# Kernel optimization log

Hardware: AMD Instinct MI355X
Metric: run time of the kernel (lower is better)

## Reference

```python
import jax, jax.numpy as jnp
import numpy as np

H, FF = 4096, 14336   # hidden size, SwiGLU intermediate size
B, S = 4, 2048        # batch, sequence length


def setup_inputs() -> dict:
    key = jax.random.key(0)
    ks = jax.random.split(key, 7)
    x = jax.random.normal(ks[0], (B, S, H), dtype=jnp.float32)
    # Ternary weights: values in {-1, 0, +1}
    gate_t = jax.random.randint(ks[1], (FF, H), -1, 2, dtype=jnp.int32)
    up_t = jax.random.randint(ks[2], (FF, H), -1, 2, dtype=jnp.int32)
    down_t = jax.random.randint(ks[3], (H, FF), -1, 2, dtype=jnp.int32)
    # Per-output-row scales (positive, realistic quantization scale magnitudes)
    gate_s = jax.random.uniform(ks[4], (FF,), jnp.float32, 0.01, 0.1)
    up_s = jax.random.uniform(ks[5], (FF,), jnp.float32, 0.01, 0.1)
    down_s = jax.random.uniform(ks[6], (H,), jnp.float32, 0.01, 0.1)
    return {"x": x, "gate_t": gate_t, "up_t": up_t, "down_t": down_t,
            "gate_s": gate_s, "up_s": up_s, "down_s": down_s}


def reference(x, gate_t, up_t, down_t, gate_s, up_s, down_s):
    # SwiGLU forward with on-the-fly ternary dequant, matching
    # TernaryExpertModule.forward (output_proj=None).
    Bb, Ss, Hh = x.shape
    x_flat = x.reshape(Bb * Ss, Hh)                         # [BS, H]
    gate_w = gate_t.astype(jnp.float32) * gate_s[:, None]   # [FF, H]
    up_w = up_t.astype(jnp.float32) * up_s[:, None]         # [FF, H]
    down_w = down_t.astype(jnp.float32) * down_s[:, None]   # [H, FF]
    gate_out = x_flat @ gate_w.T                            # [BS, FF]
    up_out = x_flat @ up_w.T                                # [BS, FF]
    hidden = jax.nn.silu(gate_out) * up_out                 # [BS, FF]
    out_flat = hidden @ down_w.T                            # [BS, H]
    return out_flat.reshape(Bb, Ss, -1)
```

## Files before the change

### kernel.cpp

```cpp
#include <hip/hip_runtime.h>
#include <stdint.h>

#define H_DIM   4096
#define FF_DIM  14336
#define M_TOK   8192
#define KC1     (H_DIM / 32)
#define KC2     (FF_DIM / 32)
#define KC1_8   (H_DIM / 64)

typedef unsigned short ushort_t;
typedef __attribute__((ext_vector_type(8))) short  bf16x8;
typedef __attribute__((ext_vector_type(4))) float  f32x4;
typedef __attribute__((ext_vector_type(4))) int    i32x4;

__device__ __forceinline__ unsigned short f2bf(float f) {
    union { float f; uint32_t u; } v; v.f = f;
    uint32_t r = v.u + 0x7FFFu + ((v.u >> 16) & 1u);
    return (unsigned short)(r >> 16);
}
__device__ __forceinline__ unsigned short t2bf(int v) {
    unsigned int mag = (v & 1) ? 0x3F80u : 0u;
    unsigned int sgn = ((unsigned int)v >> 16) & 0x8000u;
    return (unsigned short)(mag | sgn);
}
__device__ __forceinline__ bf16x8 pack_f8(f32x4 a, f32x4 b) {
    bf16x8 o;
    o[0]=(short)f2bf(a[0]); o[1]=(short)f2bf(a[1]); o[2]=(short)f2bf(a[2]); o[3]=(short)f2bf(a[3]);
    o[4]=(short)f2bf(b[0]); o[5]=(short)f2bf(b[1]); o[6]=(short)f2bf(b[2]); o[7]=(short)f2bf(b[3]);
    return o;
}
__device__ __forceinline__ bf16x8 pack_t8(i32x4 a, i32x4 b) {
    bf16x8 o;
    o[0]=(short)t2bf(a[0]); o[1]=(short)t2bf(a[1]); o[2]=(short)t2bf(a[2]); o[3]=(short)t2bf(a[3]);
    o[4]=(short)t2bf(b[0]); o[5]=(short)t2bf(b[1]); o[6]=(short)t2bf(b[2]); o[7]=(short)t2bf(b[3]);
    return o;
}
__device__ __forceinline__ int pack4(int a, int b, int c, int d) {
    return (a & 255) | ((b & 255) << 8) | ((c & 255) << 16) | ((d & 255) << 24);
}

#define GLDS16(gp, lp) __builtin_amdgcn_global_load_lds( \
    (__attribute__((address_space(1))) void*)(gp),       \
    (__attribute__((address_space(3))) void*)(lp), 16, 0, 0)

#define WAITVM8 asm volatile("s_waitcnt vmcnt(8)" ::: "memory")
#define WAITVM4 asm volatile("s_waitcnt vmcnt(4)" ::: "memory")
#define WAITVM0 asm volatile("s_waitcnt vmcnt(0)" ::: "memory")
#define SBAR    asm volatile("s_barrier" ::: "memory")


template<int K, bool TERN>
__global__ __launch_bounds__(256)
void k_cvt_lds(const void* __restrict__ inv, unsigned short* __restrict__ out) {
    constexpr int KC = K / 32;
    constexpr int CP = K / 64;
    __shared__ int sm[128][68];
    const int b   = blockIdx.x;
    const int t   = b / CP;
    const int cp  = b % CP;
    const int tid = threadIdx.x;
    const int rr  = tid >> 4;
    const int c4  = (tid & 15) * 4;
    const int k0  = cp * 64;

    const int* in = (const int*)inv;
    #pragma unroll
    for (int p = 0; p < 8; ++p) {
        const int row = p * 16 + rr;
        *(i32x4*)&sm[row][c4] = *(const i32x4*)(in + (size_t)(t * 128 + row) * K + k0 + c4);
    }
    __syncthreads();
    #pragma unroll
    for (int p = 0; p < 4; ++p) {
        const int idx = p * 256 + tid;
        const int cc  = idx >> 9;
        const int f   = (idx >> 6) & 7;
        const int l   = idx & 63;
        const int row = f * 16 + (l & 15);
        const int kl  = cc * 32 + (l >> 4) * 8;
        bf16x8 o;
        if (TERN) {
            i32x4 a = *(const i32x4*)&sm[row][kl];
            i32x4 bq = *(const i32x4*)&sm[row][kl + 4];
            o = pack_t8(a, bq);
        } else {
            f32x4 a = *(const f32x4*)&sm[row][kl];
            f32x4 bq = *(const f32x4*)&sm[row][kl + 4];
            o = pack_f8(a, bq);
        }
        *(bf16x8*)(out + (((size_t)t * KC + (cp * 2 + cc)) * 8 + f) * 512 + (size_t)l * 8) = o;
    }
}

__global__ __launch_bounds__(256)
void k_amax(const float* __restrict__ x, float* __restrict__ sx, float* __restrict__ rsx) {
    const int row  = blockIdx.x * 4 + (threadIdx.x >> 6);
    const int lane = threadIdx.x & 63;
    const f32x4* p = (const f32x4*)(x + (size_t)row * H_DIM);
    float m = 0.f;
    #pragma unroll 4
    for (int i = lane; i < H_DIM / 4; i += 64) {
        f32x4 v = p[i];
        m = fmaxf(m, fmaxf(fmaxf(fabsf(v[0]), fabsf(v[1])), fmaxf(fabsf(v[2]), fabsf(v[3]))));
    }
    #pragma unroll
    for (int o = 32; o; o >>= 1) m = fmaxf(m, __shfl_xor(m, o, 64));
    if (lane == 0) {
        sx[row]  = m * (1.f / 127.f);
        rsx[row] = m > 0.f ? 127.f / m : 0.f;
    }
}

template<int K, bool TERN>
__global__ __launch_bounds__(256)
void k_cvt_i8(const void* __restrict__ inv, const float* __restrict__ rsx,
              char* __restrict__ out) {
    constexpr int CP = K / 64;
    __shared__ int sm[128][68];
    const int b   = blockIdx.x;
    const int t   = b / CP;
    const int cp  = b % CP;
    const int tid = threadIdx.x;
    const int rr  = tid >> 4;
    const int c4  = (tid & 15) * 4;

    const int* in = (const int*)inv;
    #pragma unroll
    for (int p = 0; p < 8; ++p) {
        const int row = p * 16 + rr;
        *(i32x4*)&sm[row][c4] = *(const i32x4*)(in + (size_t)(t * 128 + row) * K + cp * 64 + c4);
    }
    __syncthreads();
    #pragma unroll
    for (int p = 0; p < 2; ++p) {
        const int pos = p * 256 + tid;
        const int f = pos >> 6, l = pos & 63;
        const int row = f * 16 + (l & 15);
        const int kb  = (l >> 4) * 16;
        i32x4 o;
        if constexpr (TERN) {
            #pragma unroll
            for (int q = 0; q < 4; ++q)
                o[q] = pack4(sm[row][kb + q * 4], sm[row][kb + q * 4 + 1],
                             sm[row][kb + q * 4 + 2], sm[row][kb + q * 4 + 3]);
        } else {
            const float rs = rsx[t * 128 + row];
            #pragma unroll
            for (int q = 0; q < 4; ++q) {
                const float* fp = (const float*)&sm[row][kb + q * 4];
                o[q] = pack4(__float2int_rn(fp[0] * rs), __float2int_rn(fp[1] * rs),
                             __float2int_rn(fp[2] * rs), __float2int_rn(fp[3] * rs));
            }
        }
        *(i32x4*)(out + ((size_t)t * CP + cp) * 8192 + f * 1024 + (size_t)l * 16) = o;
    }
}

__global__ __launch_bounds__(512, 2)
void k_gemm1_i8(const char* __restrict__ xq,
                const char* __restrict__ gq, const char* __restrict__ uq,
                const float* __restrict__ sxp,
                const float* __restrict__ gs, const float* __restrict__ us,
                ushort_t* __restrict__ hid)
{
    __shared__ char lds[131072];
    const int tid  = threadIdx.x;
    const int lane = tid & 63;
    const int wv   = tid >> 6;
    const int wr   = wv >> 1;
    const int wc   = wv & 1;
    const int l15  = lane & 15;
    const int lq   = lane >> 4;

    const int bid = blockIdx.x;
    const int bmt = bid & 31;
    const int bnt = bid >> 5;

    const char* xa0 = xq + (size_t)(bmt * 2)     * KC1_8 * 8192;
    const char* xa1 = xq + (size_t)(bmt * 2 + 1) * KC1_8 * 8192;
    const char* gbb = gq + (size_t)bnt * KC1_8 * 8192;
    const char* ubb = uq + (size_t)bnt * KC1_8 * 8192;

    i32x4 accg[4][4] = {};
    i32x4 accu[4][4] = {};

    #pragma unroll
    for (int h = 0; h < 3; ++h) {
        char* sl = lds + h * 32768;
        GLDS16(xa0 + (size_t)h * 8192 + tid * 16, sl + tid * 16);
        GLDS16(xa1 + (size_t)h * 8192 + tid * 16, sl + 8192 + tid * 16);
        GLDS16(gbb + (size_t)h * 8192 + tid * 16, sl + 16384 + tid * 16);
        GLDS16(ubb + (size_t)h * 8192 + tid * 16, sl + 24576 + tid * 16);
    }

#define G1I(WAITOP, DO_ISSUE)                                                      \
  {                                                                                \
    char* slot = lds + (H & 3) * 32768;                                            \
    const char* Ab = slot + (wr >> 1) * 8192 + ((wr & 1) * 4) * 1024 + lane * 16;  \
    const char* Gb = slot + 16384 + (wc * 4) * 1024 + lane * 16;                   \
    const char* Ub = slot + 24576 + (wc * 4) * 1024 + lane * 16;                   \
    WAITOP;                                                                        \
    SBAR;                                                                          \
    i32x4 af[4], gf[4], uf[4];                                                     \
    _Pragma("unroll")                                                              \
    for (int m = 0; m < 4; m++) af[m] = *(const i32x4*)(Ab + m * 1024);            \
    _Pragma("unroll")                                                              \
    for (int n = 0; n < 4; n++) gf[n] = *(const i32x4*)(Gb + n * 1024);            \
    if (DO_ISSUE) {                                                                \
      const int Hp = H + 3;                                                        \
      char* sp = lds + (Hp & 3) * 32768;                                           \
      GLDS16(xa0 + (size_t)Hp * 8192 + tid * 16, sp + tid * 16);                   \
      GLDS16(xa1 + (size_t)Hp * 8192 + tid * 16, sp + 8192 + tid * 16);            \
    }                                                                              \
    __builtin_amdgcn_s_setprio(1);                                                 \
    _Pragma("unroll")                                                              \
    for (int m = 0; m < 4; m++)                                                    \
      _Pragma("unroll")                                                            \
      for (int n = 0; n < 4; n++)                                                  \
        accg[m][n] = __builtin_amdgcn_mfma_i32_16x16x64_i8(af[m], gf[n], accg[m][n], 0, 0, 0); \
    __builtin_amdgcn_s_setprio(0);                                                 \
    SBAR;                                                                          \
    _Pragma("unroll")                                                              \
    for (int n = 0; n < 4; n++) uf[n] = *(const i32x4*)(Ub + n * 1024);            \
    if (DO_ISSUE) {                                                                \
      const int Hp = H + 3;                                                        \
      char* sp = lds + (Hp & 3) * 32768;                                           \
      GLDS16(gbb + (size_t)Hp * 8192 + tid * 16, sp + 16384 + tid * 16);           \
      GLDS16(ubb + (size_t)Hp * 8192 + tid * 16, sp + 24576 + tid * 16);           \
    }                                                                              \
    __builtin_amdgcn_s_setprio(1);                                                 \
    _Pragma("unroll")                                                              \
    for (int m = 0; m < 4; m++)                                                    \
      _Pragma("unroll")                                                            \
      for (int n = 0; n < 4; n++)                                                  \
        accu[m][n] = __builtin_amdgcn_mfma_i32_16x16x64_i8(af[m], uf[n], accu[m][n], 0, 0, 0); \
    __builtin_amdgcn_s_setprio(0);                                                 \
  }

    int H = 0;
    for (; H < KC1_8 - 3; ++H) G1I(WAITVM8, 1);
    G1I(WAITVM8, 0); ++H;
    G1I(WAITVM4, 0); ++H;
    G1I(WAITVM0, 0);
#undef G1I

    const int bm0 = bmt * 256;
    const int bn0 = bnt * 128;
    float sxv[4][4];
    #pragma unroll
    for (int m = 0; m < 4; m++) {
        const int rb = bm0 + wr * 64 + m * 16 + lq * 4;
        #pragma unroll
        for (int r = 0; r < 4; r++) sxv[m][r] = sxp[rb + r];
    }
    #pragma unroll
    for (int n = 0; n < 4; n++) {
        const int gcol = bn0 + wc * 64 + n * 16 + l15;
        const float sg = gs[gcol];
        const float su = us[gcol];
        const int c  = gcol >> 5;
        const int lp = ((gcol & 31) >> 3) * 16;
        const int e  = gcol & 7;
        #pragma unroll
        for (int m = 0; m < 4; m++) {
            const int rb = bm0 + wr * 64 + m * 16 + lq * 4;
            #pragma unroll
            for (int r = 0; r < 4; r++) {
                const int row = rb + r;
                float g = (float)accg[m][n][r] * (sxv[m][r] * sg);
                float u = (float)accu[m][n][r] * (sxv[m][r] * su);
                float hv = g * (1.0f / (1.0f + __expf(-g))) * u;
                const int t = row >> 7;
                const int f = (row >> 4) & 7;
                const int l = (row & 15) + lp;
                hid[(((size_t)t * KC2 + c) * 8 + f) * 512 + l * 8 + e] = f2bf(hv);
            }
        }
    }
}

__global__ __launch_bounds__(512, 2)
void k_gemm2_8p(const ushort_t* __restrict__ hid, const ushort_t* __restrict__ db,
                const float* __restrict__ dsc, float* __restrict__ out)
{
    __shared__ ushort_t lds[65536];
    const int tid  = threadIdx.x;
    const int lane = tid & 63;
    const int wv   = tid >> 6;
    const int wr   = wv >> 2;
    const int wc   = wv & 3;
    const int l15  = lane & 15;
    const int lq   = lane >> 4;

    const int bid = blockIdx.x;
    const int bmt = bid & 31;
    const int bnt = bid >> 5;

    const ushort_t* ha0 = hid + ((size_t)(bmt * 2)     * KC2) * 4096;
    const ushort_t* ha1 = hid + ((size_t)(bmt * 2 + 1) * KC2) * 4096;
    const ushort_t* db0 = db  + ((size_t)(bnt * 2)     * KC2) * 4096;
    const ushort_t* db1 = db  + ((size_t)(bnt * 2 + 1) * KC2) * 4096;

    f32x4 acc[8][4] = {};

    #pragma unroll
    for (int h = 0; h < 3; ++h) {
        ushort_t* sl = lds + h * 16384;
        GLDS16(ha0 + (size_t)h * 4096 + tid * 8, sl + tid * 8);
        GLDS16(ha1 + (size_t)h * 4096 + tid * 8, sl + 4096 + tid * 8);
        GLDS16(db0 + (size_t)h * 4096 + tid * 8, sl + 8192 + tid * 8);
        GLDS16(db1 + (size_t)h * 4096 + tid * 8, sl + 12288 + tid * 8);
    }

#define G2_HALF(WAITOP, DO_ISSUE)                                                  \
  {                                                                                \
    ushort_t* slot = lds + (H & 3) * 16384;                                        \
    const ushort_t* Ab = slot + wr * 4096 + lane * 8;                              \
    const ushort_t* Bb = slot + 8192 + (wc >> 1) * 4096 + ((wc & 1) * 4) * 512 + lane * 8; \
    WAITOP;                                                                        \
    SBAR;                                                                          \
    bf16x8 af[4], bfv[4];                                                          \
    _Pragma("unroll")                                                              \
    for (int m = 0; m < 4; m++) af[m] = *(const bf16x8*)(Ab + m * 512);            \
    _Pragma("unroll")                                                              \
    for (int n = 0; n < 4; n++) bfv[n] = *(const bf16x8*)(Bb + n * 512);           \
    if (DO_ISSUE) {                                                                \
      const int Hp = H + 3;                                                        \
      ushort_t* sp = lds + (Hp & 3) * 16384;                                       \
      GLDS16(ha0 + (size_t)Hp * 4096 + tid * 8, sp + tid * 8);                     \
      GLDS16(ha1 + (size_t)Hp * 4096 + tid * 8, sp + 4096 + tid * 8);              \
    }                                                                              \
    __builtin_amdgcn_s_setprio(1);                                                 \
    _Pragma("unroll")                                                              \
    for (int m = 0; m < 4; m++)                                                    \
      _Pragma("unroll")                                                            \
      for (int n = 0; n < 4; n++)                                                  \
        acc[m][n] = __builtin_amdgcn_mfma_f32_16x16x32_bf16(af[m], bfv[n], acc[m][n], 0, 0, 0); \
    __builtin_amdgcn_s_setprio(0);                                                 \
    SBAR;                                                                          \
    bf16x8 af2[4];                                                                 \
    _Pragma("unroll")                                                              \
    for (int m = 0; m < 4; m++) af2[m] = *(const bf16x8*)(Ab + (4 + m) * 512);     \
    if (DO_ISSUE) {                                                                \
      const int Hp = H + 3;                                                        \
      ushort_t* sp = lds + (Hp & 3) * 16384;                                       \
      GLDS16(db0 + (size_t)Hp * 4096 + tid * 8, sp + 8192 + tid * 8);              \
      GLDS16(db1 + (size_t)Hp * 4096 + tid * 8, sp + 12288 + tid * 8);             \
    }                                                                              \
    __builtin_amdgcn_s_setprio(1);                                                 \
    _Pragma("unroll")                                                              \
    for (int m = 0; m < 4; m++)                                                    \
      _Pragma("unroll")                                                            \
      for (int n = 0; n < 4; n++)                                                  \
        acc[4 + m][n] = __builtin_amdgcn_mfma_f32_16x16x32_bf16(af2[m], bfv[n], acc[4 + m][n], 0, 0, 0); \
    __builtin_amdgcn_s_setprio(0);                                                 \
  }

    int H = 0;
    for (; H < KC2 - 3; ++H) G2_HALF(WAITVM8, 1);
    G2_HALF(WAITVM8, 0); ++H;
    G2_HALF(WAITVM4, 0); ++H;
    G2_HALF(WAITVM0, 0);
#undef G2_HALF

    const int bm0 = bmt * 256;
    const int bn0 = bnt * 256;
    #pragma unroll
    for (int n = 0; n < 4; n++) {
        const int gcol = bn0 + wc * 64 + n * 16 + l15;
        const float sd = dsc[gcol];
        #pragma unroll
        for (int m = 0; m < 8; m++) {
            const int grow = bm0 + wr * 128 + m * 16 + lq * 4;
            #pragma unroll
            for (int r = 0; r < 4; r++)
                out[(size_t)(grow + r) * H_DIM + gcol] = acc[m][n][r] * sd;
        }
    }
}

__device__ __forceinline__ void ds_write_frag(ushort_t* buf, int crow, int ccol,
                                              bf16x8 lo, bf16x8 hi) {
    int f  = crow >> 4;
    int la = (crow & 15) + (((ccol)     & 31) >> 3) * 16;
    int lb = (crow & 15) + (((ccol + 8) & 31) >> 3) * 16;
    *(bf16x8*)&buf[f * 512 + la * 8] = lo;
    *(bf16x8*)&buf[f * 512 + lb * 8] = hi;
}

template<bool PREA>
__global__ __launch_bounds__(256, 2)
void k_gemm1_fb(const float* __restrict__ xf, const ushort_t* __restrict__ xb,
                const int* __restrict__ gt, const int* __restrict__ ut,
                const float* __restrict__ gs, const float* __restrict__ us,
                ushort_t* __restrict__ hid)
{
    __shared__ ushort_t As[4096];
    __shared__ ushort_t Gs[4096];
    __shared__ ushort_t Us[4096];

    const int tid  = threadIdx.x;
    const int lane = tid & 63;
    const int wv   = tid >> 6;
    const int wr   = wv >> 1;
    const int wc   = wv & 1;
    const int l15  = lane & 15;
    const int lq   = lane >> 4;

    const int bid = blockIdx.x;
    const int bmt = bid & 63;
    const int bnt = bid >> 6;
    const int bm0 = bmt * 128;
    const int bn0 = bnt * 128;

    f32x4 accg[4][4] = {};
    f32x4 accu[4][4] = {};

    const ushort_t* pa = PREA ? xb + (size_t)bmt * KC1 * 4096 : nullptr;
    const int crow = tid >> 1;
    const int ccol = (tid & 1) * 16;

    for (int kc = 0; kc < KC1; kc++) {
        __syncthreads();
        const int k0 = kc * 32;
        if constexpr (PREA) {
            GLDS16(pa + tid * 8,        &As[tid * 8]);
            GLDS16(pa + tid * 8 + 2048, &As[tid * 8 + 2048]);
        } else {
            const float* xa = xf + (size_t)(bm0 + crow) * H_DIM + k0 + ccol;
            f32x4 a0 = ((const f32x4*)xa)[0], a1 = ((const f32x4*)xa)[1];
            f32x4 a2 = ((const f32x4*)xa)[2], a3 = ((const f32x4*)xa)[3];
            ds_write_frag(As, crow, ccol, pack_f8(a0, a1), pack_f8(a2, a3));
        }
        {
            const size_t wo = (size_t)(bn0 + crow) * H_DIM + k0 + ccol;
            const i32x4* gp = (const i32x4*)(gt + wo);
            i32x4 g0 = gp[0], g1 = gp[1], g2 = gp[2], g3 = gp[3];
            ds_write_frag(Gs, crow, ccol, pack_t8(g0, g1), pack_t8(g2, g3));
            const i32x4* up = (const i32x4*)(ut + wo);
            i32x4 u0 = up[0], u1 = up[1], u2 = up[2], u3 = up[3];
            ds_write_frag(Us, crow, ccol, pack_t8(u0, u1), pack_t8(u2, u3));
        }
        __syncthreads();

        bf16x8 af[4], gf[4], uf[4];
        #pragma unroll
        for (int m = 0; m < 4; m++)
            af[m] = *(const bf16x8*)&As[(wr * 4 + m) * 512 + lane * 8];
        #pragma unroll
        for (int n = 0; n < 4; n++) {
            gf[n] = *(const bf16x8*)&Gs[(wc * 4 + n) * 512 + lane * 8];
            uf[n] = *(const bf16x8*)&Us[(wc * 4 + n) * 512 + lane * 8];
        }
        #pragma unroll
        for (int m = 0; m < 4; m++)
            #pragma unroll
            for (int n = 0; n < 4; n++) {
                accg[m][n] = __builtin_amdgcn_mfma_f32_16x16x32_bf16(af[m], gf[n], accg[m][n], 0, 0, 0);
                accu[m][n] = __builtin_amdgcn_mfma_f32_16x16x32_bf16(af[m], uf[n], accu[m][n], 0, 0, 0);
            }
        if constexpr (PREA) pa += 4096;
    }

    #pragma unroll
    for (int n = 0; n < 4; n++) {
        const int gcol = bn0 + wc * 64 + n * 16 + l15;
        const float sg = gs[gcol];
        const float su = us[gcol];
        const int c  = gcol >> 5;
        const int lp = ((gcol & 31) >> 3) * 16;
        const int e  = gcol & 7;
        #pragma unroll
        for (int m = 0; m < 4; m++) {
            const int rb = bm0 + wr * 64 + m * 16 + lq * 4;
            #pragma unroll
            for (int r = 0; r < 4; r++) {
                const int row = rb + r;
                float g = accg[m][n][r] * sg;
                float u = accu[m][n][r] * su;
                float hv = g * (1.0f / (1.0f + __expf(-g))) * u;
                const int t = row >> 7;
                const int f = (row >> 4) & 7;
                const int l = (row & 15) + lp;
                hid[(((size_t)t * KC2 + c) * 8 + f) * 512 + l * 8 + e] = f2bf(hv);
            }
        }
    }
}

__global__ __launch_bounds__(256, 2)
void k_gemm2_fb(const ushort_t* __restrict__ hid, const int* __restrict__ dt,
                const float* __restrict__ dsc, float* __restrict__ out)
{
    __shared__ ushort_t As[4096];
    __shared__ ushort_t Bs[4096];

    const int tid  = threadIdx.x;
    const int lane = tid & 63;
    const int wv   = tid >> 6;
    const int wr   = wv >> 1;
    const int wc   = wv & 1;
    const int l15  = lane & 15;
    const int lq   = lane >> 4;

    const int bid = blockIdx.x;
    const int bmt = bid & 63;
    const int bnt = bid >> 6;
    const int bm0 = bmt * 128;
    const int bn0 = bnt * 128;

    f32x4 acc[4][4] = {};
    const ushort_t* pa = hid + (size_t)bmt * KC2 * 4096;
    const int crow = tid >> 1;
    const int ccol = (tid & 1) * 16;

    for (int kc = 0; kc < KC2; kc++) {
        __syncthreads();
        GLDS16(pa + tid * 8,        &As[tid * 8]);
        GLDS16(pa + tid * 8 + 2048, &As[tid * 8 + 2048]);
        {
            const i32x4* dp = (const i32x4*)(dt + (size_t)(bn0 + crow) * FF_DIM + kc * 32 + ccol);
            i32x4 d0 = dp[0], d1 = dp[1], d2 = dp[2], d3 = dp[3];
            ds_write_frag(Bs, crow, ccol, pack_t8(d0, d1), pack_t8(d2, d3));
        }
        __syncthreads();

        bf16x8 af[4], bfr[4];
        #pragma unroll
        for (int m = 0; m < 4; m++)
            af[m] = *(const bf16x8*)&As[(wr * 4 + m) * 512 + lane * 8];
        #pragma unroll
        for (int n = 0; n < 4; n++)
            bfr[n] = *(const bf16x8*)&Bs[(wc * 4 + n) * 512 + lane * 8];
        #pragma unroll
        for (int m = 0; m < 4; m++)
            #pragma unroll
            for (int n = 0; n < 4; n++)
                acc[m][n] = __builtin_amdgcn_mfma_f32_16x16x32_bf16(af[m], bfr[n], acc[m][n], 0, 0, 0);
        pa += 4096;
    }

    #pragma unroll
    for (int n = 0; n < 4; n++) {
        const int gcol = bn0 + wc * 64 + n * 16 + l15;
        const float sd = dsc[gcol];
        #pragma unroll
        for (int m = 0; m < 4; m++) {
            const int grow = bm0 + wr * 64 + m * 16 + lq * 4;
            #pragma unroll
            for (int r = 0; r < 4; r++)
                out[(size_t)(grow + r) * H_DIM + gcol] = acc[m][n][r] * sd;
        }
    }
}

extern "C" void kernel_launch(void* const* d_in, const int* in_sizes, int n_in,
                              void* d_out, int out_size, void* d_ws, size_t ws_size,
                              hipStream_t stream) {
    const float* xf  = (const float*)d_in[0];
    const int*   gt  = (const int*)d_in[1];
    const int*   ut  = (const int*)d_in[2];
    const int*   dt  = (const int*)d_in[3];
    const float* gsc = (const float*)d_in[4];
    const float* usc = (const float*)d_in[5];
    const float* dsc = (const float*)d_in[6];
    float* out = (float*)d_out;

    const size_t HID_B = (size_t)M_TOK * FF_DIM * 2;
    const size_t DB_B  = (size_t)FF_DIM * H_DIM * 2;
    const size_t G8_B  = (size_t)FF_DIM * H_DIM;
    const size_t U8_B  = (size_t)FF_DIM * H_DIM;
    const size_t X8_B  = (size_t)M_TOK * H_DIM;
    const size_t SX_B  = (size_t)M_TOK * 4;
    const size_t XB_B  = (size_t)M_TOK * H_DIM * 2;

    char* base = (char*)d_ws;
    ushort_t* hid = (ushort_t*)base;
    ushort_t* dbp = (ushort_t*)(base + HID_B);
    char*     g8  = base + HID_B + DB_B;
    char*     u8  = g8 + G8_B;
    char*     x8  = u8 + U8_B;
    float*    sxp = (float*)(x8 + X8_B);
    float*    rsx = sxp + M_TOK;
    ushort_t* xbp = (ushort_t*)(base + HID_B);

    const bool has_w  = ws_size >= HID_B + DB_B + G8_B + U8_B + X8_B + 2 * SX_B;
    const bool has_xb = ws_size >= HID_B + XB_B;

    if (has_w) {
        k_amax<<<M_TOK / 4, 256, 0, stream>>>(xf, sxp, rsx);
        k_cvt_i8<H_DIM,  false><<<(M_TOK / 128) * (H_DIM / 64), 256, 0, stream>>>(xf, rsx, x8);
        k_cvt_i8<H_DIM,  true ><<<(FF_DIM / 128) * (H_DIM / 64), 256, 0, stream>>>(gt, nullptr, g8);
        k_cvt_i8<H_DIM,  true ><<<(FF_DIM / 128) * (H_DIM / 64), 256, 0, stream>>>(ut, nullptr, u8);
        k_cvt_lds<FF_DIM, true><<<(H_DIM / 128) * (FF_DIM / 64), 256, 0, stream>>>(dt, dbp);

        k_gemm1_i8<<<32 * 112, 512, 0, stream>>>(x8, g8, u8, sxp, gsc, usc, hid);
        k_gemm2_8p<<<32 * 16, 512, 0, stream>>>(hid, dbp, dsc, out);
    } else {
        const int grid1 = 64 * 112;
        const int grid2 = 64 * 32;
        if (has_xb) {
            k_cvt_lds<H_DIM, false><<<(M_TOK / 128) * (H_DIM / 64), 256, 0, stream>>>(xf, xbp);
            k_gemm1_fb<true><<<grid1, 256, 0, stream>>>(nullptr, xbp, gt, ut, gsc, usc, hid);
        } else {
            k_gemm1_fb<false><<<grid1, 256, 0, stream>>>(xf, nullptr, gt, ut, gsc, usc, hid);
        }
        k_gemm2_fb<<<grid2, 256, 0, stream>>>(hid, dt, dsc, out);
    }
}
```

Baseline: 1.723 ms.

## Switch gate/up int8 GEMM to 32x32x32 MFMA with matching operand layout

Replaces the 16x16x64 int8 MFMA tiles in the fused gate/up GEMM with 32x32x32 MFMA tiles. The int8 conversion kernel's packed output layout is changed to match the 32-row fragment format. The A fragments for the next k-step are prefetched from LDS into registers during the current step, and the pipeline waits on fewer outstanding loads. The aim is fewer MFMA issues and LDS reads per output, plus hiding LDS latency, at the cost of a new epilogue row mapping and per-element scale loads.

After: 1.814 ms. +5.3%, slower.

```diff
diff --git a/kernel.cpp b/kernel.cpp
--- a/kernel.cpp
+++ b/kernel.cpp
@@ -6,12 +6,14 @@
 #define M_TOK   8192
 #define KC1     (H_DIM / 32)
 #define KC2     (FF_DIM / 32)
-#define KC1_8   (H_DIM / 64)
+#define NC1     (H_DIM / 64)
+#define CPX     (H_DIM / 32)
 
 typedef unsigned short ushort_t;
-typedef __attribute__((ext_vector_type(8))) short  bf16x8;
-typedef __attribute__((ext_vector_type(4))) float  f32x4;
-typedef __attribute__((ext_vector_type(4))) int    i32x4;
+typedef __attribute__((ext_vector_type(8)))  short bf16x8;
+typedef __attribute__((ext_vector_type(4)))  float f32x4;
+typedef __attribute__((ext_vector_type(4)))  int   i32x4;
+typedef __attribute__((ext_vector_type(16))) int   i32x16;
 
 __device__ __forceinline__ unsigned short f2bf(float f) {
     union { float f; uint32_t u; } v; v.f = f;
@@ -115,11 +117,11 @@
 __global__ __launch_bounds__(256)
 void k_cvt_i8(const void* __restrict__ inv, const float* __restrict__ rsx,
               char* __restrict__ out) {
-    constexpr int CP = K / 64;
+    constexpr int CP = K / 32;
     __shared__ int sm[128][68];
     const int b   = blockIdx.x;
-    const int t   = b / CP;
-    const int cp  = b % CP;
+    const int t   = b / (K / 64);
+    const int cp  = b % (K / 64);
     const int tid = threadIdx.x;
     const int rr  = tid >> 4;
     const int c4  = (tid & 15) * 4;
@@ -134,9 +136,11 @@
     #pragma unroll
     for (int p = 0; p < 2; ++p) {
         const int pos = p * 256 + tid;
-        const int f = pos >> 6, l = pos & 63;
-        const int row = f * 16 + (l & 15);
-        const int kb  = (l >> 4) * 16;
+        const int cc  = pos >> 8;
+        const int f   = (pos >> 6) & 3;
+        const int l   = pos & 63;
+        const int row = f * 32 + (l & 31);
+        const int kb  = cc * 32 + (l >> 5) * 16;
         i32x4 o;
         if constexpr (TERN) {
             #pragma unroll
@@ -152,7 +156,7 @@
                              __float2int_rn(fp[2] * rs), __float2int_rn(fp[3] * rs));
             }
         }
-        *(i32x4*)(out + ((size_t)t * CP + cp) * 8192 + f * 1024 + (size_t)l * 16) = o;
+        *(i32x4*)(out + ((size_t)(t * CP + cp * 2 + cc) * 4 + f) * 1024 + (size_t)l * 16) = o;
     }
 }
 
@@ -169,106 +173,111 @@
     const int wv   = tid >> 6;
     const int wr   = wv >> 1;
     const int wc   = wv & 1;
-    const int l15  = lane & 15;
-    const int lq   = lane >> 4;
+    const int l31  = lane & 31;
+    const int lhi  = lane >> 5;
 
     const int bid = blockIdx.x;
     const int bmt = bid & 31;
     const int bnt = bid >> 5;
 
-    const char* xa0 = xq + (size_t)(bmt * 2)     * KC1_8 * 8192;
-    const char* xa1 = xq + (size_t)(bmt * 2 + 1) * KC1_8 * 8192;
-    const char* gbb = gq + (size_t)bnt * KC1_8 * 8192;
-    const char* ubb = uq + (size_t)bnt * KC1_8 * 8192;
-
-    i32x4 accg[4][4] = {};
-    i32x4 accu[4][4] = {};
-
-    #pragma unroll
-    for (int h = 0; h < 3; ++h) {
-        char* sl = lds + h * 32768;
-        GLDS16(xa0 + (size_t)h * 8192 + tid * 16, sl + tid * 16);
-        GLDS16(xa1 + (size_t)h * 8192 + tid * 16, sl + 8192 + tid * 16);
-        GLDS16(gbb + (size_t)h * 8192 + tid * 16, sl + 16384 + tid * 16);
-        GLDS16(ubb + (size_t)h * 8192 + tid * 16, sl + 24576 + tid * 16);
-    }
-
-#define G1I(WAITOP, DO_ISSUE)                                                      \
-  {                                                                                \
-    char* slot = lds + (H & 3) * 32768;                                            \
-    const char* Ab = slot + (wr >> 1) * 8192 + ((wr & 1) * 4) * 1024 + lane * 16;  \
-    const char* Gb = slot + 16384 + (wc * 4) * 1024 + lane * 16;                   \
-    const char* Ub = slot + 24576 + (wc * 4) * 1024 + lane * 16;                   \
-    WAITOP;                                                                        \
-    SBAR;                                                                          \
-    i32x4 af[4], gf[4], uf[4];                                                     \
-    _Pragma("unroll")                                                              \
-    for (int m = 0; m < 4; m++) af[m] = *(const i32x4*)(Ab + m * 1024);            \
-    _Pragma("unroll")                                                              \
-    for (int n = 0; n < 4; n++) gf[n] = *(const i32x4*)(Gb + n * 1024);            \
-    if (DO_ISSUE) {                                                                \
-      const int Hp = H + 3;                                                        \
-      char* sp = lds + (Hp & 3) * 32768;                                           \
-      GLDS16(xa0 + (size_t)Hp * 8192 + tid * 16, sp + tid * 16);                   \
-      GLDS16(xa1 + (size_t)Hp * 8192 + tid * 16, sp + 8192 + tid * 16);            \
-    }                                                                              \
-    __builtin_amdgcn_s_setprio(1);                                                 \
-    _Pragma("unroll")                                                              \
-    for (int m = 0; m < 4; m++)                                                    \
-      _Pragma("unroll")                                                            \
-      for (int n = 0; n < 4; n++)                                                  \
-        accg[m][n] = __builtin_amdgcn_mfma_i32_16x16x64_i8(af[m], gf[n], accg[m][n], 0, 0, 0); \
-    __builtin_amdgcn_s_setprio(0);                                                 \
-    SBAR;                                                                          \
-    _Pragma("unroll")                                                              \
-    for (int n = 0; n < 4; n++) uf[n] = *(const i32x4*)(Ub + n * 1024);            \
-    if (DO_ISSUE) {                                                                \
-      const int Hp = H + 3;                                                        \
-      char* sp = lds + (Hp & 3) * 32768;                                           \
-      GLDS16(gbb + (size_t)Hp * 8192 + tid * 16, sp + 16384 + tid * 16);           \
-      GLDS16(ubb + (size_t)Hp * 8192 + tid * 16, sp + 24576 + tid * 16);           \
-    }                                                                              \
-    __builtin_amdgcn_s_setprio(1);                                                 \
-    _Pragma("unroll")                                                              \
-    for (int m = 0; m < 4; m++)                                                    \
-      _Pragma("unroll")                                                            \
-      for (int n = 0; n < 4; n++)                                                  \
-        accu[m][n] = __builtin_amdgcn_mfma_i32_16x16x64_i8(af[m], uf[n], accu[m][n], 0, 0, 0); \
-    __builtin_amdgcn_s_setprio(0);                                                 \
+    const char* xa0  = xq + (size_t)(2 * bmt)     * CPX * 4096;
+    const char* xa1  = xq + (size_t)(2 * bmt + 1) * CPX * 4096;
+    const char* srcA = (tid < 256 ? xa0 : xa1 - 4096) + tid * 16;
+    const char* gbb  = gq + (size_t)bnt * CPX * 4096;
+    const char* ubb  = uq + (size_t)bnt * CPX * 4096;
+
+    i32x16 accg[2][2] = {};
+    i32x16 accu[2][2] = {};
+    i32x4  af[2][2], afn[2][2];
+
+#define STAGE1(h) { char* sl_ = lds + ((h) & 3) * 32768;                     \
+    GLDS16(srcA + (size_t)(h) * 8192,           sl_ + tid * 16);             \
+    GLDS16(srcA + (size_t)(h) * 8192 + 4096,    sl_ + 8192  + tid * 16);     \
+    GLDS16(gbb  + (size_t)(h) * 8192 + tid * 16, sl_ + 16384 + tid * 16);    \
+    GLDS16(ubb  + (size_t)(h) * 8192 + tid * 16, sl_ + 24576 + tid * 16); }
+
+    STAGE1(0); STAGE1(1); STAGE1(2);
+    WAITVM8;
+    SBAR;
+    #pragma unroll
+    for (int c2 = 0; c2 < 2; ++c2)
+        #pragma unroll
+        for (int i = 0; i < 2; ++i)
+            af[c2][i] = *(const i32x4*)(lds + c2 * 8192 + (wr * 2 + i) * 1024 + lane * 16);
+
+#define G1BODY(WAITOP, DO_STAGE, DO_AFN)                                            \
+  {                                                                                 \
+    char* slot = lds + (H & 3) * 32768;                                             \
+    WAITOP;                                              \
+    SBAR;               \
+    if (DO_STAGE) STAGE1(H + 3);                                                    \
+    i32x4 gf[2][2], uf[2][2];                                                       \
+    _Pragma("unroll")                                                               \
+    for (int c2 = 0; c2 < 2; ++c2)                                                  \
+      _Pragma("unroll")                                                             \
+      for (int n = 0; n < 2; ++n) {                                                 \
+        gf[c2][n] = *(const i32x4*)(slot + 16384 + c2 * 4096 + (wc * 2 + n) * 1024 + lane * 16); \
+        uf[c2][n] = *(const i32x4*)(slot + 24576 + c2 * 4096 + (wc * 2 + n) * 1024 + lane * 16); \
+      }                                                                             \
+    if (DO_AFN) {                                                                   \
+      char* sn = lds + ((H + 1) & 3) * 32768;                                       \
+      _Pragma("unroll")                                                             \
+      for (int c2 = 0; c2 < 2; ++c2)                                                \
+        _Pragma("unroll")                                                           \
+        for (int i = 0; i < 2; ++i)                                                 \
+          afn[c2][i] = *(const i32x4*)(sn + c2 * 8192 + (wr * 2 + i) * 1024 + lane * 16); \
+    }                                                                               \
+    __builtin_amdgcn_s_setprio(1);                                                  \
+    _Pragma("unroll")                                                               \
+    for (int c2 = 0; c2 < 2; ++c2)                                                  \
+      _Pragma("unroll")                                                             \
+      for (int i = 0; i < 2; ++i)                                                   \
+        _Pragma("unroll")                                                           \
+        for (int n = 0; n < 2; ++n)                                                 \
+          accg[i][n] = __builtin_amdgcn_mfma_i32_32x32x32_i8(af[c2][i], gf[c2][n], accg[i][n], 0, 0, 0); \
+    _Pragma("unroll")                                                               \
+    for (int c2 = 0; c2 < 2; ++c2)                                                  \
+      _Pragma("unroll")                                                             \
+      for (int i = 0; i < 2; ++i)                                                   \
+        _Pragma("unroll")                                                           \
+        for (int n = 0; n < 2; ++n)                                                 \
+          accu[i][n] = __builtin_amdgcn_mfma_i32_32x32x32_i8(af[c2][i], uf[c2][n], accu[i][n], 0, 0, 0); \
+    __builtin_amdgcn_s_setprio(0);                                                  \
+    if (DO_AFN) {                                                                   \
+      _Pragma("unroll")                                                             \
+      for (int c2 = 0; c2 < 2; ++c2)                                                \
+        _Pragma("unroll")                                                           \
+        for (int i = 0; i < 2; ++i) af[c2][i] = afn[c2][i];                         \
+    }                                                                               \
   }
 
     int H = 0;
-    for (; H < KC1_8 - 3; ++H) G1I(WAITVM8, 1);
-    G1I(WAITVM8, 0); ++H;
-    G1I(WAITVM4, 0); ++H;
-    G1I(WAITVM0, 0);
-#undef G1I
+    for (; H < NC1 - 3; ++H) G1BODY(WAITVM4, 1, 1);
+    G1BODY(WAITVM4, 0, 1); ++H;
+    G1BODY(WAITVM0, 0, 1); ++H;
+    G1BODY(WAITVM0, 0, 0);
+#undef G1BODY
+#undef STAGE1
 
     const int bm0 = bmt * 256;
     const int bn0 = bnt * 128;
-    float sxv[4][4];
-    #pragma unroll
-    for (int m = 0; m < 4; m++) {
-        const int rb = bm0 + wr * 64 + m * 16 + lq * 4;
-        #pragma unroll
-        for (int r = 0; r < 4; r++) sxv[m][r] = sxp[rb + r];
-    }
-    #pragma unroll
-    for (int n = 0; n < 4; n++) {
-        const int gcol = bn0 + wc * 64 + n * 16 + l15;
-        const float sg = gs[gcol];
-        const float su = us[gcol];
-        const int c  = gcol >> 5;
-        const int lp = ((gcol & 31) >> 3) * 16;
-        const int e  = gcol & 7;
-        #pragma unroll
-        for (int m = 0; m < 4; m++) {
-            const int rb = bm0 + wr * 64 + m * 16 + lq * 4;
-            #pragma unroll
-            for (int r = 0; r < 4; r++) {
-                const int row = rb + r;
-                float g = (float)accg[m][n][r] * (sxv[m][r] * sg);
-                float u = (float)accu[m][n][r] * (sxv[m][r] * su);
+    #pragma unroll
+    for (int i = 0; i < 2; ++i) {
+        #pragma unroll
+        for (int n = 0; n < 2; ++n) {
+            const int col = bn0 + wc * 64 + n * 32 + l31;
+            const float sg = gs[col];
+            const float su = us[col];
+            const int c  = col >> 5;
+            const int lp = ((col & 31) >> 3) * 16;
+            const int e  = col & 7;
+            #pragma unroll
+            for (int reg = 0; reg < 16; ++reg) {
+                const int row32 = (reg & 3) + 8 * (reg >> 2) + 4 * lhi;
+                const int row = bm0 + wr * 64 + i * 32 + row32;
+                const float sx = sxp[row];
+                float g = (float)accg[i][n][reg] * (sx * sg);
+                float u = (float)accu[i][n][reg] * (sx * su);
                 float hv = g * (1.0f / (1.0f + __expf(-g))) * u;
                 const int t = row >> 7;
                 const int f = (row >> 4) & 7;
```

## Switch gemm1 int8 pipeline from 4-slot triple-prefetch to double buffering

Applied to the files above, without the earlier changes.

Replaces the four-slot LDS ring, which prefetched three K-chunks ahead and split the issue of x and gate/up loads across two barrier phases, with a two-slot double buffer that prefetches one chunk ahead. LDS use halves to 64 KB, which could let more blocks fit per CU alongside the 512-thread launch bounds of 2. The cost is a shallower prefetch distance, so global-memory latency is hidden less, plus a trailing barrier added each iteration.

Measured after the change: 1.778 ms. 3.2% more time.

```diff
diff --git a/kernel.cpp b/kernel.cpp
--- a/kernel.cpp
+++ b/kernel.cpp
@@ -6,12 +6,12 @@
 #define M_TOK   8192
 #define KC1     (H_DIM / 32)
 #define KC2     (FF_DIM / 32)
-#define KC1_8   (H_DIM / 64)
+#define NC1     (H_DIM / 64)
 
 typedef unsigned short ushort_t;
-typedef __attribute__((ext_vector_type(8))) short  bf16x8;
-typedef __attribute__((ext_vector_type(4))) float  f32x4;
-typedef __attribute__((ext_vector_type(4))) int    i32x4;
+typedef __attribute__((ext_vector_type(8)))  short bf16x8;
+typedef __attribute__((ext_vector_type(4)))  float f32x4;
+typedef __attribute__((ext_vector_type(4)))  int   i32x4;
 
 __device__ __forceinline__ unsigned short f2bf(float f) {
     union { float f; uint32_t u; } v; v.f = f;
@@ -43,10 +43,10 @@
     (__attribute__((address_space(1))) void*)(gp),       \
     (__attribute__((address_space(3))) void*)(lp), 16, 0, 0)
 
-#define WAITVM8 asm volatile("s_waitcnt vmcnt(8)" ::: "memory")
-#define WAITVM4 asm volatile("s_waitcnt vmcnt(4)" ::: "memory")
-#define WAITVM0 asm volatile("s_waitcnt vmcnt(0)" ::: "memory")
-#define SBAR    asm volatile("s_barrier" ::: "memory")
+#define WAITVM8  asm volatile("s_waitcnt vmcnt(8)" ::: "memory")
+#define WAITVM4  asm volatile("s_waitcnt vmcnt(4)" ::: "memory")
+#define WAITVM0  asm volatile("s_waitcnt vmcnt(0)" ::: "memory")
+#define SBAR     asm volatile("s_barrier" ::: "memory")
 
 
 template<int K, bool TERN>
@@ -163,7 +163,7 @@
                 const float* __restrict__ gs, const float* __restrict__ us,
                 ushort_t* __restrict__ hid)
 {
-    __shared__ char lds[131072];
+    __shared__ char lds[65536];
     const int tid  = threadIdx.x;
     const int lane = tid & 63;
     const int wv   = tid >> 6;
@@ -176,73 +176,58 @@
     const int bmt = bid & 31;
     const int bnt = bid >> 5;
 
-    const char* xa0 = xq + (size_t)(bmt * 2)     * KC1_8 * 8192;
-    const char* xa1 = xq + (size_t)(bmt * 2 + 1) * KC1_8 * 8192;
-    const char* gbb = gq + (size_t)bnt * KC1_8 * 8192;
-    const char* ubb = uq + (size_t)bnt * KC1_8 * 8192;
+    const char* xa0 = xq + (size_t)(bmt * 2)     * NC1 * 8192;
+    const char* xa1 = xq + (size_t)(bmt * 2 + 1) * NC1 * 8192;
+    const char* gbb = gq + (size_t)bnt * NC1 * 8192;
+    const char* ubb = uq + (size_t)bnt * NC1 * 8192;
 
     i32x4 accg[4][4] = {};
     i32x4 accu[4][4] = {};
 
-    #pragma unroll
-    for (int h = 0; h < 3; ++h) {
-        char* sl = lds + h * 32768;
-        GLDS16(xa0 + (size_t)h * 8192 + tid * 16, sl + tid * 16);
-        GLDS16(xa1 + (size_t)h * 8192 + tid * 16, sl + 8192 + tid * 16);
-        GLDS16(gbb + (size_t)h * 8192 + tid * 16, sl + 16384 + tid * 16);
-        GLDS16(ubb + (size_t)h * 8192 + tid * 16, sl + 24576 + tid * 16);
-    }
-
-#define G1I(WAITOP, DO_ISSUE)                                                      \
-  {                                                                                \
-    char* slot = lds + (H & 3) * 32768;                                            \
-    const char* Ab = slot + (wr >> 1) * 8192 + ((wr & 1) * 4) * 1024 + lane * 16;  \
-    const char* Gb = slot + 16384 + (wc * 4) * 1024 + lane * 16;                   \
-    const char* Ub = slot + 24576 + (wc * 4) * 1024 + lane * 16;                   \
-    WAITOP;                                                                        \
-    SBAR;                                                                          \
-    i32x4 af[4], gf[4], uf[4];                                                     \
-    _Pragma("unroll")                                                              \
-    for (int m = 0; m < 4; m++) af[m] = *(const i32x4*)(Ab + m * 1024);            \
-    _Pragma("unroll")                                                              \
-    for (int n = 0; n < 4; n++) gf[n] = *(const i32x4*)(Gb + n * 1024);            \
-    if (DO_ISSUE) {                                                                \
-      const int Hp = H + 3;                                                        \
-      char* sp = lds + (Hp & 3) * 32768;                                           \
-      GLDS16(xa0 + (size_t)Hp * 8192 + tid * 16, sp + tid * 16);                   \
-      GLDS16(xa1 + (size_t)Hp * 8192 + tid * 16, sp + 8192 + tid * 16);            \
-    }                                                                              \
-    __builtin_amdgcn_s_setprio(1);                                                 \
-    _Pragma("unroll")                                                              \
-    for (int m = 0; m < 4; m++)                                                    \
-      _Pragma("unroll")                                                            \
-      for (int n = 0; n < 4; n++)                                                  \
+#define STAGE1(h) { char* sl_ = lds + ((h) & 1) * 32768;                     \
+    GLDS16(xa0 + (size_t)(h) * 8192 + tid * 16, sl_ + tid * 16);             \
+    GLDS16(xa1 + (size_t)(h) * 8192 + tid * 16, sl_ + 8192  + tid * 16);     \
+    GLDS16(gbb + (size_t)(h) * 8192 + tid * 16, sl_ + 16384 + tid * 16);     \
+    GLDS16(ubb + (size_t)(h) * 8192 + tid * 16, sl_ + 24576 + tid * 16); }
+
+#define G1BODY(WAITOP, DO_STAGE)                                                    \
+  {                                                                                 \
+    if (DO_STAGE) STAGE1(H + 1);                                                    \
+    WAITOP;              \
+    SBAR;                                        \
+    char* slot = lds + (H & 1) * 32768;                                             \
+    const char* Ab = slot + (wr >> 1) * 8192 + ((wr & 1) * 4) * 1024 + lane * 16;   \
+    const char* Gb = slot + 16384 + (wc * 4) * 1024 + lane * 16;                    \
+    const char* Ub = slot + 24576 + (wc * 4) * 1024 + lane * 16;                    \
+    i32x4 af[4], gf[4], uf[4];                                                      \
+    _Pragma("unroll")                                                               \
+    for (int m = 0; m < 4; m++) af[m] = *(const i32x4*)(Ab + m * 1024);             \
+    _Pragma("unroll")                                                               \
+    for (int n = 0; n < 4; n++) {                                                   \
+        gf[n] = *(const i32x4*)(Gb + n * 1024);                                     \
+        uf[n] = *(const i32x4*)(Ub + n * 1024);                                     \
+    }                                                                               \
+    __builtin_amdgcn_s_setprio(1);                                                  \
+    _Pragma("unroll")                                                               \
+    for (int m = 0; m < 4; m++)                                                     \
+      _Pragma("unroll")                                                             \
+      for (int n = 0; n < 4; n++)                                                   \
         accg[m][n] = __builtin_amdgcn_mfma_i32_16x16x64_i8(af[m], gf[n], accg[m][n], 0, 0, 0); \
-    __builtin_amdgcn_s_setprio(0);                                                 \
-    SBAR;                                                                          \
-    _Pragma("unroll")                                                              \
-    for (int n = 0; n < 4; n++) uf[n] = *(const i32x4*)(Ub + n * 1024);            \
-    if (DO_ISSUE) {                                                                \
-      const int Hp = H + 3;                                                        \
-      char* sp = lds + (Hp & 3) * 32768;                                           \
-      GLDS16(gbb + (size_t)Hp * 8192 + tid * 16, sp + 16384 + tid * 16);           \
-      GLDS16(ubb + (size_t)Hp * 8192 + tid * 16, sp + 24576 + tid * 16);           \
-    }                                                                              \
-    __builtin_amdgcn_s_setprio(1);                                                 \
-    _Pragma("unroll")                                                              \
-    for (int m = 0; m < 4; m++)                                                    \
-      _Pragma("unroll")                                                            \
-      for (int n = 0; n < 4; n++)                                                  \
+    _Pragma("unroll")                                                               \
+    for (int m = 0; m < 4; m++)                                                     \
+      _Pragma("unroll")                                                             \
+      for (int n = 0; n < 4; n++)                                                   \
         accu[m][n] = __builtin_amdgcn_mfma_i32_16x16x64_i8(af[m], uf[n], accu[m][n], 0, 0, 0); \
-    __builtin_amdgcn_s_setprio(0);                                                 \
+    __builtin_amdgcn_s_setprio(0);                                                  \
+    SBAR;                \
   }
 
+    STAGE1(0);
     int H = 0;
-    for (; H < KC1_8 - 3; ++H) G1I(WAITVM8, 1);
-    G1I(WAITVM8, 0); ++H;
-    G1I(WAITVM4, 0); ++H;
-    G1I(WAITVM0, 0);
-#undef G1I
+    for (; H < NC1 - 1; ++H) G1BODY(WAITVM4, 1);
+    G1BODY(WAITVM0, 0);
+#undef G1BODY
+#undef STAGE1
 
     const int bm0 = bmt * 256;
     const int bn0 = bnt * 128;
```
